# Optimization experiments

Hardware: AMD Instinct MI355X
Metric: run time of the kernel (lower is better)

## Reference

```python
import jax, jax.numpy as jnp
import numpy as np

T, B, E, H = 512, 64, 1024, 1024


def setup_inputs() -> dict:
    key = jax.random.key(0)
    ks = jax.random.split(key, 9)
    s = 1.0 / np.sqrt(E + H)  # torch Linear default init scale
    def lin(kw, kb):
        W = jax.random.uniform(kw, (H, E + H), jnp.float32, -s, s)
        b = jax.random.uniform(kb, (H,), jnp.float32, -s, s)
        return W, b
    Wf, bf = lin(ks[0], ks[1])
    Wi, bi = lin(ks[2], ks[3])
    Wo, bo = lin(ks[4], ks[5])
    Wc, bc = lin(ks[6], ks[7])
    embedding = jax.random.normal(ks[8], (T, B, E), jnp.float32)
    return {"embedding": embedding, "Wf": Wf, "bf": bf, "Wi": Wi, "bi": bi,
            "Wo": Wo, "bo": bo, "Wc": Wc, "bc": bc}


def reference(embedding, Wf, bf, Wi, bi, Wo, bo, Wc, bc):
    # embedding: [T, B, E]; each W: [H, E+H] acting on concat([x, h]).
    t, b, e = embedding.shape
    h_dim = bf.shape[0]
    # Fuse the 4 gate linears into one GEMM; split input vs hidden parts.
    Wx = jnp.concatenate([Wf[:, :e], Wi[:, :e], Wo[:, :e], Wc[:, :e]], axis=0)   # [4H, E]
    Wh = jnp.concatenate([Wf[:, e:], Wi[:, e:], Wo[:, e:], Wc[:, e:]], axis=0)   # [4H, H]
    bias = jnp.concatenate([bf, bi, bo, bc])                                      # [4H]
    # Precompute input contribution for all timesteps in one big GEMM.
    xg = jnp.einsum('tbe,ge->tbg', embedding, Wx) + bias                          # [T, B, 4H]

    def step(carry, xg_t):
        h, c = carry
        g = xg_t + h @ Wh.T                                                       # [B, 4H]
        f = jax.nn.sigmoid(g[:, :h_dim])
        i = jax.nn.sigmoid(g[:, h_dim:2 * h_dim])
        o = jax.nn.sigmoid(g[:, 2 * h_dim:3 * h_dim])
        c_tilde = jnp.tanh(g[:, 3 * h_dim:])
        c_new = f * c + i * c_tilde
        h_new = o * jnp.tanh(c_new)
        return (h_new, c_new), h_new

    h0 = jnp.zeros((b, h_dim), embedding.dtype)
    c0 = jnp.zeros((b, h_dim), embedding.dtype)
    _, hs = jax.lax.scan(step, (h0, c0), xg)                                      # [T, B, H]
    return jnp.transpose(hs, (1, 0, 2))                                           # [B, T, H] (torch.stack dim=1)
```

## Files before the change

### kernel.cpp

```cpp
#include <hip/hip_runtime.h>
#include <stdint.h>

#define T_DIM 512
#define B_DIM 64
#define E_DIM 1024
#define H_DIM 1024
#define G_DIM 4096
#define SBLK 256
#define CPB  64

typedef short bf16x8 __attribute__((ext_vector_type(8)));
typedef float f32x4 __attribute__((ext_vector_type(4)));

__device__ __forceinline__ unsigned short f2b(float f){
  union{float f; unsigned u;} v; v.f = f;
  unsigned r = (v.u + 0x7FFFu + ((v.u >> 16) & 1u)) >> 16;
  return (unsigned short)r;
}
__device__ __forceinline__ float b2f(unsigned short u){
  union{unsigned u; float f;} v; v.u = ((unsigned)u) << 16; return v.f;
}
__device__ __forceinline__ float fsigmoid(float x){
  return 1.f / (1.f + __expf(-x));
}
__device__ __forceinline__ float ftanh(float x){
  return 2.f / (1.f + __expf(-2.f * x)) - 1.f;
}

template<int OFF>
__device__ __forceinline__ bf16x8 ld_h16(const unsigned short* p){
  bf16x8 r;
  asm volatile("global_load_dwordx4 %0, %1, off offset:%2 sc0 sc1"
               : "=v"(r) : "v"(p), "i"(OFF) : "memory");
  return r;
}
__device__ __forceinline__ bf16x8 ld_g16(const unsigned short* p){
  bf16x8 r;
  asm volatile("global_load_dwordx4 %0, %1, off"
               : "=v"(r) : "v"(p) : "memory");
  return r;
}

#define LD8(dst, base, K0) \
  dst[0]=ld_h16<((K0)+0)*64>(base); dst[1]=ld_h16<((K0)+1)*64>(base); \
  dst[2]=ld_h16<((K0)+2)*64>(base); dst[3]=ld_h16<((K0)+3)*64>(base); \
  dst[4]=ld_h16<((K0)+4)*64>(base); dst[5]=ld_h16<((K0)+5)*64>(base); \
  dst[6]=ld_h16<((K0)+6)*64>(base); dst[7]=ld_h16<((K0)+7)*64>(base);

#define WAITV(N) \
  asm volatile("s_waitcnt vmcnt(" #N ")" ::: "memory"); \
  __builtin_amdgcn_sched_barrier(0x100);

#define MFMA_GRP(buf, G) \
  { _Pragma("unroll") \
    for (int u = 0; u < 8; ++u){ \
      int kc_ = (G)*8 + u; \
      bf16x8 b0 = *(const bf16x8*)&Wl[((0*32 + kc_)*64 + lane)*8]; \
      bf16x8 b1 = *(const bf16x8*)&Wl[((1*32 + kc_)*64 + lane)*8]; \
      bf16x8 b2 = *(const bf16x8*)&Wl[((2*32 + kc_)*64 + lane)*8]; \
      bf16x8 b3 = *(const bf16x8*)&Wl[((3*32 + kc_)*64 + lane)*8]; \
      acc0 = __builtin_amdgcn_mfma_f32_16x16x32_bf16(buf[u], b0, acc0, 0,0,0); \
      acc1 = __builtin_amdgcn_mfma_f32_16x16x32_bf16(buf[u], b1, acc1, 0,0,0); \
      acc2 = __builtin_amdgcn_mfma_f32_16x16x32_bf16(buf[u], b2, acc2, 0,0,0); \
      acc3 = __builtin_amdgcn_mfma_f32_16x16x32_bf16(buf[u], b3, acc3, 0,0,0); \
    } }


__global__ void pack_weights(const float* __restrict__ Wf, const float* __restrict__ Wi,
                             const float* __restrict__ Wo, const float* __restrict__ Wc,
                             const float* __restrict__ bfv, const float* __restrict__ biv,
                             const float* __restrict__ bov, const float* __restrict__ bcv,
                             unsigned short* __restrict__ WxB, unsigned short* __restrict__ WhB,
                             float* __restrict__ biasP){
  int p = blockIdx.x;
  int j = p >> 2, g = p & 3;
  const float* W    = (g==0)?Wf:(g==1)?Wi:(g==2)?Wo:Wc;
  const float* bsrc = (g==0)?bfv:(g==1)?biv:(g==2)?bov:bcv;
  const float* wrow = W + (size_t)j * 2048;
  int t = threadIdx.x;
  float4 x = *(const float4*)(wrow + 4*t);
  float4 h = *(const float4*)(wrow + 1024 + 4*t);
  ushort4 xo = make_ushort4(f2b(x.x), f2b(x.y), f2b(x.z), f2b(x.w));
  ushort4 ho = make_ushort4(f2b(h.x), f2b(h.y), f2b(h.z), f2b(h.w));
  *(ushort4*)&WxB[(size_t)p*1024 + 4*t] = xo;
  *(ushort4*)&WhB[(size_t)p*1024 + 4*t] = ho;
  if (t == 0) biasP[p] = bsrc[j];
}

__global__ void conv_emb(const float* __restrict__ emb, unsigned short* __restrict__ embB,
                         size_t n4){
  for (size_t i = (size_t)blockIdx.x * blockDim.x + threadIdx.x; i < n4;
       i += (size_t)gridDim.x * blockDim.x){
    float4 v = ((const float4*)emb)[i];
    ((ushort4*)embB)[i] = make_ushort4(f2b(v.x), f2b(v.y), f2b(v.z), f2b(v.w));
  }
}

__global__ void zero_state(unsigned short* __restrict__ h0, unsigned short* __restrict__ h1,
                           float* __restrict__ c, int* __restrict__ flags){
  int i = blockIdx.x * blockDim.x + threadIdx.x;
  h0[i] = 0; h1[i] = 0; c[i] = 0.f;
  if (i < SBLK * 16) flags[i] = 0;
}

__launch_bounds__(256)
__global__ void gemm_xg(const unsigned short* __restrict__ A,
                        const unsigned short* __restrict__ B,
                        unsigned short* __restrict__ C){
  __shared__ unsigned short Al[128*32];
  __shared__ unsigned short Bl[128*32];
  int m0 = blockIdx.x * 128, n0 = blockIdx.y * 128;
  int tid = threadIdx.x, lane = tid & 63, wid = tid >> 6;
  int mblk = (wid >> 1) * 64, nblk = (wid & 1) * 64;
  int rl = lane & 15, kg = lane >> 4;
  f32x4 acc[4][4] = {};

  for (int kk = 0; kk < 1024; kk += 32){
    {
      int c0 = tid, c1 = tid + 256;
      int r = c0 >> 2, g = c0 & 3, s = g ^ ((r >> 1) & 3);
      *(uint4*)&Al[r*32 + s*8] = *(const uint4*)&A[(size_t)(m0 + r)*1024 + kk + g*8];
      *(uint4*)&Bl[r*32 + s*8] = *(const uint4*)&B[(size_t)(n0 + r)*1024 + kk + g*8];
      r = c1 >> 2; g = c1 & 3; s = g ^ ((r >> 1) & 3);
      *(uint4*)&Al[r*32 + s*8] = *(const uint4*)&A[(size_t)(m0 + r)*1024 + kk + g*8];
      *(uint4*)&Bl[r*32 + s*8] = *(const uint4*)&B[(size_t)(n0 + r)*1024 + kk + g*8];
    }
    __syncthreads();
    bf16x8 a[4], b[4];
    #pragma unroll
    for (int mf = 0; mf < 4; ++mf){
      int r = mblk + mf*16 + rl;
      a[mf] = *(const bf16x8*)&Al[r*32 + (kg ^ ((r >> 1) & 3))*8];
    }
    #pragma unroll
    for (int nf = 0; nf < 4; ++nf){
      int r = nblk + nf*16 + rl;
      b[nf] = *(const bf16x8*)&Bl[r*32 + (kg ^ ((r >> 1) & 3))*8];
    }
    #pragma unroll
    for (int mf = 0; mf < 4; ++mf)
      #pragma unroll
      for (int nf = 0; nf < 4; ++nf)
        acc[mf][nf] = __builtin_amdgcn_mfma_f32_16x16x32_bf16(a[mf], b[nf], acc[mf][nf], 0, 0, 0);
    __syncthreads();
  }

  int rq = kg * 4;
  #pragma unroll
  for (int mf = 0; mf < 4; ++mf)
    #pragma unroll
    for (int nf = 0; nf < 4; ++nf){
      int col = n0 + nblk + nf*16 + rl;
      #pragma unroll
      for (int r = 0; r < 4; ++r){
        int row = m0 + mblk + mf*16 + rq + r;
        C[(size_t)row * G_DIM + col] = f2b(acc[mf][nf][r]);
      }
    }
}

__launch_bounds__(64, 1)
__global__ void lstm_scan(const unsigned short* __restrict__ WhB,
                          const unsigned short* __restrict__ xgc,
                          const float* __restrict__ biasP,
                          unsigned short* __restrict__ hb0,
                          unsigned short* __restrict__ hb1,
                          float* __restrict__ cglob,
                          float* __restrict__ out,
                          int* __restrict__ flags,
                          int t0, int t1){
  __shared__ unsigned short Wl[4*32*64*8];
  __shared__ float gl[16][68];

  const int tid = threadIdx.x;
  const int blk = blockIdx.x;
  const int cs = blk >> 2, rq = blk & 3;
  const int lane = tid;
  const int rl = lane & 15, kg = lane >> 4;

  for (int idx = tid; idx < 4*32*64; idx += 64){
    int ct = idx >> 11, kc = (idx >> 6) & 31, l = idx & 63;
    int col = cs*CPB + ct*16 + (l & 15);
    int k   = kc*32 + (l >> 4)*8;
    *(bf16x8*)&Wl[idx*8] = *(const bf16x8*)&WhB[(size_t)col*1024 + k];
  }

  const int bb = tid >> 2, q = tid & 3, cb = q * 16;
  const int rowg = rq*16 + bb;
  const int jb = cs*16 + q*4;
  f32x4 bias[4];
  #pragma unroll
  for (int p = 0; p < 4; ++p)
    bias[p] = *(const f32x4*)&biasP[cs*CPB + cb + p*4];
  f32x4 cv = *(const f32x4*)&cglob[(size_t)rowg*H_DIM + jb];

  const int* fpoll = &flags[(4*lane + rq) * 16];

  __syncthreads();
  asm volatile("s_waitcnt vmcnt(0)" ::: "memory");

  for (int t = t0; t < t1; ++t){
    const unsigned short* hin = (t & 1) ? hb1 : hb0;
    unsigned short* hout = (t & 1) ? hb0 : hb1;

    const unsigned short* xgp = xgc + ((size_t)(t - t0)*B_DIM + rowg)*G_DIM + cs*CPB + cb;
    const unsigned short* ap  = hin + (size_t)(rq*16 + rl)*1024 + kg*8;
    bf16x8 xr0 = ld_g16(xgp);
    bf16x8 xr1 = ld_g16(xgp + 8);
    bf16x8 aA[8], aB[8], aC[8], aD[8];
    LD8(aA, ap, 0);  LD8(aB, ap, 8);  LD8(aC, ap, 16);  LD8(aD, ap, 24);

    f32x4 acc0 = {}, acc1 = {}, acc2 = {}, acc3 = {};
    WAITV(24);
    MFMA_GRP(aA, 0);
    WAITV(16);
    MFMA_GRP(aB, 1);
    WAITV(8);
    MFMA_GRP(aC, 2);
    WAITV(0);
    MFMA_GRP(aD, 3);

    {
      int r0 = kg * 4;
      #pragma unroll
      for (int r = 0; r < 4; ++r){
        gl[r0 + r][ 0 + rl] = acc0[r];
        gl[r0 + r][16 + rl] = acc1[r];
        gl[r0 + r][32 + rl] = acc2[r];
        gl[r0 + r][48 + rl] = acc3[r];
      }
    }
    __syncthreads();

    union { ushort4 s; unsigned long long qq; } hu;
    f32x4 ov;
    {
      f32x4 g0, g1, g2, g3;
      #pragma unroll
      for (int e = 0; e < 4; ++e){
        g0[e] = gl[bb][cb +  0 + e] + b2f(xr0[e])     + bias[0][e];
        g1[e] = gl[bb][cb +  4 + e] + b2f(xr0[4 + e]) + bias[1][e];
        g2[e] = gl[bb][cb +  8 + e] + b2f(xr1[e])     + bias[2][e];
        g3[e] = gl[bb][cb + 12 + e] + b2f(xr1[4 + e]) + bias[3][e];
      }
      float f, i_, o, ct_, hn;
      f = fsigmoid(g0[0]); i_ = fsigmoid(g0[1]); o = fsigmoid(g0[2]); ct_ = ftanh(g0[3]);
      cv[0] = f*cv[0] + i_*ct_; hn = o*ftanh(cv[0]); hu.s.x = f2b(hn); ov[0] = hn;
      f = fsigmoid(g1[0]); i_ = fsigmoid(g1[1]); o = fsigmoid(g1[2]); ct_ = ftanh(g1[3]);
      cv[1] = f*cv[1] + i_*ct_; hn = o*ftanh(cv[1]); hu.s.y = f2b(hn); ov[1] = hn;
      f = fsigmoid(g2[0]); i_ = fsigmoid(g2[1]); o = fsigmoid(g2[2]); ct_ = ftanh(g2[3]);
      cv[2] = f*cv[2] + i_*ct_; hn = o*ftanh(cv[2]); hu.s.z = f2b(hn); ov[2] = hn;
      f = fsigmoid(g3[0]); i_ = fsigmoid(g3[1]); o = fsigmoid(g3[2]); ct_ = ftanh(g3[3]);
      cv[3] = f*cv[3] + i_*ct_; hn = o*ftanh(cv[3]); hu.s.w = f2b(hn); ov[3] = hn;
    }
    __hip_atomic_store((unsigned long long*)&hout[(size_t)rowg*H_DIM + jb], hu.qq,
                       __ATOMIC_RELAXED, __HIP_MEMORY_SCOPE_AGENT);
    *(f32x4*)&out[((size_t)rowg*T_DIM + t)*H_DIM + jb] = ov;

    if (t + 1 < t1){
      asm volatile("s_waitcnt vmcnt(0)" ::: "memory");
      __syncthreads();
      if (tid == 0)
        __hip_atomic_store(&flags[blk * 16], t + 1,
                           __ATOMIC_RELAXED, __HIP_MEMORY_SCOPE_AGENT);
      {
        const int target = t + 1;
        while (__hip_atomic_load(fpoll, __ATOMIC_RELAXED, __HIP_MEMORY_SCOPE_AGENT) < target)
          __builtin_amdgcn_s_sleep(1);
      }
      __syncthreads();
      asm volatile("" ::: "memory");
    }
  }

  *(f32x4*)&cglob[(size_t)rowg*H_DIM + jb] = cv;
}

__device__ __forceinline__ bf16x8 cvt_f8(const float* p){
  float4 u = *(const float4*)p;
  float4 v = *(const float4*)(p + 4);
  bf16x8 r;
  r[0] = (short)f2b(u.x); r[1] = (short)f2b(u.y); r[2] = (short)f2b(u.z); r[3] = (short)f2b(u.w);
  r[4] = (short)f2b(v.x); r[5] = (short)f2b(v.y); r[6] = (short)f2b(v.z); r[7] = (short)f2b(v.w);
  return r;
}

__launch_bounds__(256)
__global__ void lstm_step(const unsigned short* __restrict__ WhB,
                          const unsigned short* __restrict__ WxB,
                          const float* __restrict__ emb_t,
                          const unsigned short* __restrict__ h_in,
                          unsigned short* __restrict__ h_out,
                          float* __restrict__ cbuf,
                          const float* __restrict__ biasP,
                          float* __restrict__ out, int t){
  __shared__ float glds[64 * 17];
  int tid = threadIdx.x, lane = tid & 63, w = tid >> 6;
  int blk = blockIdx.x;
  int rl = lane & 15, kg = lane >> 4;
  int arow = w * 16 + rl;
  int pcol = blk * 16 + rl;

  f32x4 acc0 = {}, acc1 = {};
  const unsigned short* hrow = h_in + (size_t)arow * 1024 + kg * 8;
  const unsigned short* wrow = WhB + (size_t)pcol * 1024 + kg * 8;
  #pragma unroll 4
  for (int kk = 0; kk < 1024; kk += 64){
    bf16x8 a0 = *(const bf16x8*)(hrow + kk);
    bf16x8 b0 = *(const bf16x8*)(wrow + kk);
    bf16x8 a1 = *(const bf16x8*)(hrow + kk + 32);
    bf16x8 b1 = *(const bf16x8*)(wrow + kk + 32);
    acc0 = __builtin_amdgcn_mfma_f32_16x16x32_bf16(a0, b0, acc0, 0, 0, 0);
    acc1 = __builtin_amdgcn_mfma_f32_16x16x32_bf16(a1, b1, acc1, 0, 0, 0);
  }
  {
    const float* xrow = emb_t + (size_t)arow * 1024 + kg * 8;
    const unsigned short* wxrow = WxB + (size_t)pcol * 1024 + kg * 8;
    #pragma unroll 4
    for (int kk = 0; kk < 1024; kk += 64){
      bf16x8 a0 = cvt_f8(xrow + kk);
      bf16x8 b0 = *(const bf16x8*)(wxrow + kk);
      bf16x8 a1 = cvt_f8(xrow + kk + 32);
      bf16x8 b1 = *(const bf16x8*)(wxrow + kk + 32);
      acc0 = __builtin_amdgcn_mfma_f32_16x16x32_bf16(a0, b0, acc0, 0, 0, 0);
      acc1 = __builtin_amdgcn_mfma_f32_16x16x32_bf16(a1, b1, acc1, 0, 0, 0);
    }
  }
  f32x4 acc = acc0 + acc1;

  #pragma unroll
  for (int r = 0; r < 4; ++r){
    int brow = w * 16 + kg * 4 + r;
    glds[brow * 17 + rl] = acc[r];
  }
  __syncthreads();

  int b = tid >> 2, jj = tid & 3;
  int j = blk * 4 + jj;
  int pbase = blk * 16 + jj * 4;
  float gf = glds[b*17 + jj*4 + 0] + biasP[pbase + 0];
  float gi = glds[b*17 + jj*4 + 1] + biasP[pbase + 1];
  float go = glds[b*17 + jj*4 + 2] + biasP[pbase + 2];
  float gc = glds[b*17 + jj*4 + 3] + biasP[pbase + 3];
  float f  = fsigmoid(gf);
  float i_ = fsigmoid(gi);
  float o  = fsigmoid(go);
  float ct = ftanh(gc);
  float c_old = cbuf[b * H_DIM + j];
  float cn = f * c_old + i_ * ct;
  float hn = o * ftanh(cn);
  cbuf[b * H_DIM + j] = cn;
  h_out[b * H_DIM + j] = f2b(hn);
  out[((size_t)b * T_DIM + t) * H_DIM + j] = hn;
}

extern "C" void kernel_launch(void* const* d_in, const int* in_sizes, int n_in,
                              void* d_out, int out_size, void* d_ws, size_t ws_size,
                              hipStream_t stream){
  (void)in_sizes; (void)n_in; (void)out_size;
  const float* emb = (const float*)d_in[0];
  const float* Wf  = (const float*)d_in[1];
  const float* bfv = (const float*)d_in[2];
  const float* Wi  = (const float*)d_in[3];
  const float* biv = (const float*)d_in[4];
  const float* Wo  = (const float*)d_in[5];
  const float* bov = (const float*)d_in[6];
  const float* Wc  = (const float*)d_in[7];
  const float* bcv = (const float*)d_in[8];
  float* out = (float*)d_out;

  char* ws = (char*)d_ws;
  size_t off = 0;
  auto alloc = [&](size_t bytes) -> void* {
    void* p = ws + off; off += (bytes + 255) & ~(size_t)255; return p;
  };
  unsigned short* WxB   = (unsigned short*)alloc((size_t)G_DIM * 1024 * 2);
  unsigned short* WhB   = (unsigned short*)alloc((size_t)G_DIM * 1024 * 2);
  float*          biasP = (float*)alloc((size_t)G_DIM * 4);
  unsigned short* h0    = (unsigned short*)alloc((size_t)B_DIM * H_DIM * 2);
  unsigned short* h1    = (unsigned short*)alloc((size_t)B_DIM * H_DIM * 2);
  float*          cglob = (float*)alloc((size_t)B_DIM * H_DIM * 4);
  int*            flags = (int*)alloc((size_t)SBLK * 16 * 4);
  size_t base_end = off;

  int Tc = 0;
  const int cands[6] = {512, 256, 128, 64, 32, 16};
  for (int ci = 0; ci < 6; ++ci){
    size_t need = base_end
                + (size_t)cands[ci] * B_DIM * E_DIM * 2
                + (size_t)cands[ci] * B_DIM * G_DIM * 2
                + 4096;
    if (ws_size >= need){ Tc = cands[ci]; break; }
  }
  unsigned short* embB = nullptr;
  unsigned short* xgc  = nullptr;
  if (Tc > 0){
    embB = (unsigned short*)alloc((size_t)Tc * B_DIM * E_DIM * 2);
    xgc  = (unsigned short*)alloc((size_t)Tc * B_DIM * G_DIM * 2);
  }

  pack_weights<<<G_DIM, 256, 0, stream>>>(Wf, Wi, Wo, Wc, bfv, biv, bov, bcv, WxB, WhB, biasP);
  zero_state<<<256, 256, 0, stream>>>(h0, h1, cglob, flags);

  if (Tc > 0){
    for (int t0 = 0; t0 < T_DIM; t0 += Tc){
      conv_emb<<<2048, 256, 0, stream>>>(emb + (size_t)t0 * B_DIM * E_DIM, embB,
                                         (size_t)Tc * B_DIM * E_DIM / 4);
      gemm_xg<<<dim3(Tc * B_DIM / 128, G_DIM / 128), 256, 0, stream>>>(embB, WxB, xgc);
      lstm_scan<<<SBLK, 64, 0, stream>>>(WhB, xgc, biasP, h0, h1, cglob, out,
                                         flags, t0, t0 + Tc);
    }
  } else {
    for (int t = 0; t < T_DIM; ++t){
      const unsigned short* hin = (t & 1) ? h1 : h0;
      unsigned short*      hout = (t & 1) ? h0 : h1;
      lstm_step<<<256, 256, 0, stream>>>(
          WhB, WxB, emb + (size_t)t * B_DIM * E_DIM, hin, hout, cglob, biasP, out, t);
    }
  }
}
```

Before: 2.966 ms.

## Replace flag barrier with sentinel-tagged triple-buffered hidden state polling

Removes the per-step flag store/poll barrier between blocks. Hidden state is kept in a triple buffer whose slots are pre-filled with a bf16 sentinel, and consumers spin-reload only the h chunks that still hold the sentinel, so data arrival itself serves as the signal. Each block also resets its slice of the next buffer to the sentinel, and the xg loads for the next step are issued early. The aim is to cut cross-block synchronisation latency on the serial recurrence. The cost is extra polling reloads, and correctness depends on no real h value ever equalling the sentinel pattern and on ordering across the three buffers. Initial state handling when T is split into chunks also looks fragile, since only the first two buffers are seeded with the sentinel.

```diff
diff --git a/kernel.cpp b/kernel.cpp
--- a/kernel.cpp
+++ b/kernel.cpp
@@ -12,6 +12,9 @@
 typedef short bf16x8 __attribute__((ext_vector_type(8)));
 typedef float f32x4 __attribute__((ext_vector_type(4)));
 
+#define SENT16 0xFF80u
+#define SENT64 0xFF80FF80FF80FF80ULL
+
 __device__ __forceinline__ unsigned short f2b(float f){
   union{float f; unsigned u;} v; v.f = f;
   unsigned r = (v.u + 0x7FFFu + ((v.u >> 16) & 1u)) >> 16;
@@ -41,15 +44,22 @@
   return r;
 }
 
-#define LD8(dst, base, K0) \
-  dst[0]=ld_h16<((K0)+0)*64>(base); dst[1]=ld_h16<((K0)+1)*64>(base); \
-  dst[2]=ld_h16<((K0)+2)*64>(base); dst[3]=ld_h16<((K0)+3)*64>(base); \
-  dst[4]=ld_h16<((K0)+4)*64>(base); dst[5]=ld_h16<((K0)+5)*64>(base); \
-  dst[6]=ld_h16<((K0)+6)*64>(base); dst[7]=ld_h16<((K0)+7)*64>(base);
-
-#define WAITV(N) \
-  asm volatile("s_waitcnt vmcnt(" #N ")" ::: "memory"); \
-  __builtin_amdgcn_sched_barrier(0x100);
+#define RELOAD8(mask, dst, base, K0) \
+  if(((mask)>>0)&1u) dst[0]=ld_h16<((K0)+0)*64>(base); \
+  if(((mask)>>1)&1u) dst[1]=ld_h16<((K0)+1)*64>(base); \
+  if(((mask)>>2)&1u) dst[2]=ld_h16<((K0)+2)*64>(base); \
+  if(((mask)>>3)&1u) dst[3]=ld_h16<((K0)+3)*64>(base); \
+  if(((mask)>>4)&1u) dst[4]=ld_h16<((K0)+4)*64>(base); \
+  if(((mask)>>5)&1u) dst[5]=ld_h16<((K0)+5)*64>(base); \
+  if(((mask)>>6)&1u) dst[6]=ld_h16<((K0)+6)*64>(base); \
+  if(((mask)>>7)&1u) dst[7]=ld_h16<((K0)+7)*64>(base);
+
+#define CHECK8(mask, dst) { \
+  mask = 0; \
+  _Pragma("unroll") \
+  for (int f_ = 0; f_ < 8; ++f_) \
+    mask |= (unsigned)(((unsigned short)dst[f_][0]) == SENT16 || \
+                       ((unsigned short)dst[f_][4]) == SENT16) << f_; }
 
 #define MFMA_GRP(buf, G) \
   { _Pragma("unroll") \
@@ -96,11 +106,14 @@
   }
 }
 
-__global__ void zero_state(unsigned short* __restrict__ h0, unsigned short* __restrict__ h1,
-                           float* __restrict__ c, int* __restrict__ flags){
+__global__ void zero_state(unsigned short* __restrict__ hbuf,
+                           float* __restrict__ c, int scan_mode){
   int i = blockIdx.x * blockDim.x + threadIdx.x;
-  h0[i] = 0; h1[i] = 0; c[i] = 0.f;
-  if (i < SBLK * 16) flags[i] = 0;
+  unsigned short s = scan_mode ? (unsigned short)SENT16 : (unsigned short)0;
+  hbuf[i] = s;
+  hbuf[i + B_DIM*H_DIM] = s;
+  hbuf[i + 2*B_DIM*H_DIM] = 0;
+  c[i] = 0.f;
 }
 
 __launch_bounds__(256)
@@ -163,11 +176,9 @@
 __global__ void lstm_scan(const unsigned short* __restrict__ WhB,
                           const unsigned short* __restrict__ xgc,
                           const float* __restrict__ biasP,
-                          unsigned short* __restrict__ hb0,
-                          unsigned short* __restrict__ hb1,
+                          unsigned short* __restrict__ hbuf,
                           float* __restrict__ cglob,
                           float* __restrict__ out,
-                          int* __restrict__ flags,
                           int t0, int t1){
   __shared__ unsigned short Wl[4*32*64*8];
   __shared__ float gl[16][68];
@@ -194,30 +205,40 @@
     bias[p] = *(const f32x4*)&biasP[cs*CPB + cb + p*4];
   f32x4 cv = *(const f32x4*)&cglob[(size_t)rowg*H_DIM + jb];
 
-  const int* fpoll = &flags[(4*lane + rq) * 16];
-
   __syncthreads();
-  asm volatile("s_waitcnt vmcnt(0)" ::: "memory");
+
+  const unsigned short* xgp0 = xgc + ((size_t)0*B_DIM + rowg)*G_DIM + cs*CPB + cb;
+  bf16x8 xr0 = ld_g16(xgp0);
+  bf16x8 xr1 = ld_g16(xgp0 + 8);
 
   for (int t = t0; t < t1; ++t){
-    const unsigned short* hin = (t & 1) ? hb1 : hb0;
-    unsigned short* hout = (t & 1) ? hb0 : hb1;
-
-    const unsigned short* xgp = xgc + ((size_t)(t - t0)*B_DIM + rowg)*G_DIM + cs*CPB + cb;
-    const unsigned short* ap  = hin + (size_t)(rq*16 + rl)*1024 + kg*8;
-    bf16x8 xr0 = ld_g16(xgp);
-    bf16x8 xr1 = ld_g16(xgp + 8);
+    const unsigned short* hin  = hbuf + (size_t)((t + 2) % 3) * B_DIM * H_DIM;
+    unsigned short*       hout = hbuf + (size_t)( t      % 3) * B_DIM * H_DIM;
+    unsigned short*       hrst = hbuf + (size_t)((t + 1) % 3) * B_DIM * H_DIM;
+
+    const unsigned short* ap = hin + (size_t)(rq*16 + rl)*1024 + kg*8;
     bf16x8 aA[8], aB[8], aC[8], aD[8];
-    LD8(aA, ap, 0);  LD8(aB, ap, 8);  LD8(aC, ap, 16);  LD8(aD, ap, 24);
+    unsigned mA = 0xFFu, mB = 0xFFu, mC = 0xFFu, mD = 0xFFu;
+    for (int pass = 0; pass < 8192; ++pass){
+      RELOAD8(mA, aA, ap, 0);
+      RELOAD8(mB, aB, ap, 8);
+      RELOAD8(mC, aC, ap, 16);
+      RELOAD8(mD, aD, ap, 24);
+      asm volatile("s_waitcnt vmcnt(0)" ::: "memory");
+      __builtin_amdgcn_sched_barrier(0);
+      CHECK8(mA, aA); CHECK8(mB, aB); CHECK8(mC, aC); CHECK8(mD, aD);
+      if (!__any((mA | mB | mC | mD) != 0u)) break;
+      __builtin_amdgcn_s_sleep(1);
+    }
+
+    __hip_atomic_store(
+        (unsigned long long*)&hrst[(size_t)(rq*16 + rl)*H_DIM + cs*16 + kg*4],
+        SENT64, __ATOMIC_RELAXED, __HIP_MEMORY_SCOPE_AGENT);
 
     f32x4 acc0 = {}, acc1 = {}, acc2 = {}, acc3 = {};
-    WAITV(24);
     MFMA_GRP(aA, 0);
-    WAITV(16);
     MFMA_GRP(aB, 1);
-    WAITV(8);
     MFMA_GRP(aC, 2);
-    WAITV(0);
     MFMA_GRP(aD, 3);
 
     {
@@ -253,24 +274,17 @@
       f = fsigmoid(g3[0]); i_ = fsigmoid(g3[1]); o = fsigmoid(g3[2]); ct_ = ftanh(g3[3]);
       cv[3] = f*cv[3] + i_*ct_; hn = o*ftanh(cv[3]); hu.s.w = f2b(hn); ov[3] = hn;
     }
+
+    asm volatile("s_waitcnt vmcnt(0)" ::: "memory");
     __hip_atomic_store((unsigned long long*)&hout[(size_t)rowg*H_DIM + jb], hu.qq,
                        __ATOMIC_RELAXED, __HIP_MEMORY_SCOPE_AGENT);
     *(f32x4*)&out[((size_t)rowg*T_DIM + t)*H_DIM + jb] = ov;
-
     if (t + 1 < t1){
-      asm volatile("s_waitcnt vmcnt(0)" ::: "memory");
-      __syncthreads();
-      if (tid == 0)
-        __hip_atomic_store(&flags[blk * 16], t + 1,
-                           __ATOMIC_RELAXED, __HIP_MEMORY_SCOPE_AGENT);
-      {
-        const int target = t + 1;
-        while (__hip_atomic_load(fpoll, __ATOMIC_RELAXED, __HIP_MEMORY_SCOPE_AGENT) < target)
-          __builtin_amdgcn_s_sleep(1);
-      }
-      __syncthreads();
-      asm volatile("" ::: "memory");
-    }
+      const unsigned short* xgp = xgc + ((size_t)(t + 1 - t0)*B_DIM + rowg)*G_DIM + cs*CPB + cb;
+      xr0 = ld_g16(xgp);
+      xr1 = ld_g16(xgp + 8);
+    }
+    __syncthreads();
   }
 
   *(f32x4*)&cglob[(size_t)rowg*H_DIM + jb] = cv;
@@ -377,10 +391,8 @@
   unsigned short* WxB   = (unsigned short*)alloc((size_t)G_DIM * 1024 * 2);
   unsigned short* WhB   = (unsigned short*)alloc((size_t)G_DIM * 1024 * 2);
   float*          biasP = (float*)alloc((size_t)G_DIM * 4);
-  unsigned short* h0    = (unsigned short*)alloc((size_t)B_DIM * H_DIM * 2);
-  unsigned short* h1    = (unsigned short*)alloc((size_t)B_DIM * H_DIM * 2);
+  unsigned short* hbuf  = (unsigned short*)alloc((size_t)3 * B_DIM * H_DIM * 2);
   float*          cglob = (float*)alloc((size_t)B_DIM * H_DIM * 4);
-  int*            flags = (int*)alloc((size_t)SBLK * 16 * 4);
   size_t base_end = off;
 
   int Tc = 0;
@@ -400,17 +412,19 @@
   }
 
   pack_weights<<<G_DIM, 256, 0, stream>>>(Wf, Wi, Wo, Wc, bfv, biv, bov, bcv, WxB, WhB, biasP);
-  zero_state<<<256, 256, 0, stream>>>(h0, h1, cglob, flags);
+  zero_state<<<256, 256, 0, stream>>>(hbuf, cglob, Tc > 0 ? 1 : 0);
 
   if (Tc > 0){
     for (int t0 = 0; t0 < T_DIM; t0 += Tc){
       conv_emb<<<2048, 256, 0, stream>>>(emb + (size_t)t0 * B_DIM * E_DIM, embB,
                                          (size_t)Tc * B_DIM * E_DIM / 4);
       gemm_xg<<<dim3(Tc * B_DIM / 128, G_DIM / 128), 256, 0, stream>>>(embB, WxB, xgc);
-      lstm_scan<<<SBLK, 64, 0, stream>>>(WhB, xgc, biasP, h0, h1, cglob, out,
-                                         flags, t0, t0 + Tc);
+      lstm_scan<<<SBLK, 64, 0, stream>>>(WhB, xgc, biasP, hbuf, cglob, out,
+                                         t0, t0 + Tc);
     }
   } else {
+    unsigned short* h0 = hbuf;
+    unsigned short* h1 = hbuf + (size_t)B_DIM * H_DIM;
     for (int t = 0; t < T_DIM; ++t){
       const unsigned short* hin = (t & 1) ? h1 : h0;
       unsigned short*      hout = (t & 1) ? h0 : h1;
```

Measured after the change: 3.763 ms. 1.27x slower.

## Restructure LSTM scan into 64 blocks with two-phase batch-half pipelining

Applied to the files above, without the earlier changes.

The persistent scan kernel now runs 64 blocks instead of 256. Each block covers all 64 batch rows, split into two halves of 32 that alternate phases, so one half's MFMA work overlaps the other half's flag wait and prefetch of h and xg. The block-wide barrier plus single flag is replaced by per-half flags, wave-level __any polling, and non-blocking flag prefetch, with asm-level stores and tuned vmcnt waits. This is meant to cut grid-wide synchronisation cost and expose latency hiding across the recurrence. The cost is fewer CUs in use and fragile hand-counted waitcnt sequencing.

```diff
diff --git a/kernel.cpp b/kernel.cpp
--- a/kernel.cpp
+++ b/kernel.cpp
@@ -6,7 +6,7 @@
 #define E_DIM 1024
 #define H_DIM 1024
 #define G_DIM 4096
-#define SBLK 256
+#define SBLK 64
 #define CPB  64
 
 typedef short bf16x8 __attribute__((ext_vector_type(8)));
@@ -40,18 +40,40 @@
                : "=v"(r) : "v"(p) : "memory");
   return r;
 }
-
-#define LD8(dst, base, K0) \
-  dst[0]=ld_h16<((K0)+0)*64>(base); dst[1]=ld_h16<((K0)+1)*64>(base); \
-  dst[2]=ld_h16<((K0)+2)*64>(base); dst[3]=ld_h16<((K0)+3)*64>(base); \
-  dst[4]=ld_h16<((K0)+4)*64>(base); dst[5]=ld_h16<((K0)+5)*64>(base); \
-  dst[6]=ld_h16<((K0)+6)*64>(base); dst[7]=ld_h16<((K0)+7)*64>(base);
+__device__ __forceinline__ void st_h16(unsigned short* p, bf16x8 v){
+  asm volatile("global_store_dwordx4 %0, %1, off sc0 sc1"
+               :: "v"(p), "v"(v) : "memory");
+}
+__device__ __forceinline__ void st_g16(float* p, f32x4 v){
+  asm volatile("global_store_dwordx4 %0, %1, off"
+               :: "v"(p), "v"(v) : "memory");
+}
+__device__ __forceinline__ void st_flag(int* p, int v){
+  asm volatile("global_store_dword %0, %1, off sc0 sc1"
+               :: "v"(p), "v"(v) : "memory");
+}
+__device__ __forceinline__ int ld_flag_nb(const int* p){
+  int r;
+  asm volatile("global_load_dword %0, %1, off sc0 sc1"
+               : "=v"(r) : "v"(p) : "memory");
+  return r;
+}
 
 #define WAITV(N) \
   asm volatile("s_waitcnt vmcnt(" #N ")" ::: "memory"); \
   __builtin_amdgcn_sched_barrier(0x100);
 
-#define MFMA_GRP(buf, G) \
+#define LD16(d0, d1, p0, p1, G) \
+  d0[0]=ld_h16<((G)*8+0)*64>(p0); d0[1]=ld_h16<((G)*8+1)*64>(p0); \
+  d0[2]=ld_h16<((G)*8+2)*64>(p0); d0[3]=ld_h16<((G)*8+3)*64>(p0); \
+  d0[4]=ld_h16<((G)*8+4)*64>(p0); d0[5]=ld_h16<((G)*8+5)*64>(p0); \
+  d0[6]=ld_h16<((G)*8+6)*64>(p0); d0[7]=ld_h16<((G)*8+7)*64>(p0); \
+  d1[0]=ld_h16<((G)*8+0)*64>(p1); d1[1]=ld_h16<((G)*8+1)*64>(p1); \
+  d1[2]=ld_h16<((G)*8+2)*64>(p1); d1[3]=ld_h16<((G)*8+3)*64>(p1); \
+  d1[4]=ld_h16<((G)*8+4)*64>(p1); d1[5]=ld_h16<((G)*8+5)*64>(p1); \
+  d1[6]=ld_h16<((G)*8+6)*64>(p1); d1[7]=ld_h16<((G)*8+7)*64>(p1);
+
+#define MFMA_GRP2(a0, a1, G) \
   { _Pragma("unroll") \
     for (int u = 0; u < 8; ++u){ \
       int kc_ = (G)*8 + u; \
@@ -59,10 +81,14 @@
       bf16x8 b1 = *(const bf16x8*)&Wl[((1*32 + kc_)*64 + lane)*8]; \
       bf16x8 b2 = *(const bf16x8*)&Wl[((2*32 + kc_)*64 + lane)*8]; \
       bf16x8 b3 = *(const bf16x8*)&Wl[((3*32 + kc_)*64 + lane)*8]; \
-      acc0 = __builtin_amdgcn_mfma_f32_16x16x32_bf16(buf[u], b0, acc0, 0,0,0); \
-      acc1 = __builtin_amdgcn_mfma_f32_16x16x32_bf16(buf[u], b1, acc1, 0,0,0); \
-      acc2 = __builtin_amdgcn_mfma_f32_16x16x32_bf16(buf[u], b2, acc2, 0,0,0); \
-      acc3 = __builtin_amdgcn_mfma_f32_16x16x32_bf16(buf[u], b3, acc3, 0,0,0); \
+      acc00 = __builtin_amdgcn_mfma_f32_16x16x32_bf16(a0[u], b0, acc00, 0,0,0); \
+      acc01 = __builtin_amdgcn_mfma_f32_16x16x32_bf16(a0[u], b1, acc01, 0,0,0); \
+      acc02 = __builtin_amdgcn_mfma_f32_16x16x32_bf16(a0[u], b2, acc02, 0,0,0); \
+      acc03 = __builtin_amdgcn_mfma_f32_16x16x32_bf16(a0[u], b3, acc03, 0,0,0); \
+      acc10 = __builtin_amdgcn_mfma_f32_16x16x32_bf16(a1[u], b0, acc10, 0,0,0); \
+      acc11 = __builtin_amdgcn_mfma_f32_16x16x32_bf16(a1[u], b1, acc11, 0,0,0); \
+      acc12 = __builtin_amdgcn_mfma_f32_16x16x32_bf16(a1[u], b2, acc12, 0,0,0); \
+      acc13 = __builtin_amdgcn_mfma_f32_16x16x32_bf16(a1[u], b3, acc13, 0,0,0); \
     } }
 
 
@@ -100,7 +126,7 @@
                            float* __restrict__ c, int* __restrict__ flags){
   int i = blockIdx.x * blockDim.x + threadIdx.x;
   h0[i] = 0; h1[i] = 0; c[i] = 0.f;
-  if (i < SBLK * 16) flags[i] = 0;
+  if (i < 4096) flags[i] = 0;
 }
 
 __launch_bounds__(256)
@@ -159,6 +185,70 @@
     }
 }
 
+#define PHASE(G, t)                                                            \
+{                                                                              \
+             \
+  WAITV(18);        \
+  st_flag(&flags[(cs*2 + ((G)^1))*16], ((G)==0) ? (t) : ((t)+1));              \
+  f32x4 acc00={},acc01={},acc02={},acc03={},acc10={},acc11={},acc12={},acc13={};\
+  MFMA_GRP2(P0, P1, 0);                                                        \
+  LD16(P0, P1, ap0, ap1, 2);                    \
+  LD16(R0, R1, ap0, ap1, 3);                                                   \
+  pv = ld_flag_nb(&flags[(lane*2 + ((G)^1))*16]);                              \
+  WAITV(35);                                                \
+  MFMA_GRP2(Q0, Q1, 1);                                                        \
+  WAITV(17);                                                \
+  MFMA_GRP2(P0, P1, 2);                                                        \
+  WAITV(1);                               \
+  MFMA_GRP2(R0, R1, 3);                                                        \
+  asm volatile("s_waitcnt lgkmcnt(0)" ::: "memory");                           \
+  { int r0 = kg*4;                                                             \
+    _Pragma("unroll") for (int rg = 0; rg < 4; ++rg){                          \
+      gl[r0+rg][ 0+rl]=acc00[rg]; gl[r0+rg][16+rl]=acc01[rg];                  \
+      gl[r0+rg][32+rl]=acc02[rg]; gl[r0+rg][48+rl]=acc03[rg];                  \
+      gl[16+r0+rg][ 0+rl]=acc10[rg]; gl[16+r0+rg][16+rl]=acc11[rg];            \
+      gl[16+r0+rg][32+rl]=acc12[rg]; gl[16+r0+rg][48+rl]=acc13[rg]; } }        \
+  asm volatile("s_waitcnt lgkmcnt(0)" ::: "memory");                           \
+  __builtin_amdgcn_sched_barrier(0);                                           \
+  union{ unsigned short us[8]; bf16x8 v; } hp;                                 \
+  f32x4 ovA, ovB;                                                              \
+  _Pragma("unroll") for (int m = 0; m < 8; ++m){                               \
+    f32x4 gv = *(const f32x4*)&gl[bb][q*32 + m*4];                             \
+    _Pragma("unroll") for (int e = 0; e < 4; ++e)                              \
+      gv[e] += b2f((unsigned short)xr[m>>1][(m&1)*4 + e]) + bias8[m][e];       \
+    float f_ = fsigmoid(gv[0]), i_ = fsigmoid(gv[1]);                          \
+    float o_ = fsigmoid(gv[2]), ct_ = ftanh(gv[3]);                            \
+    float c_ = f_*cvs[G][m] + i_*ct_; cvs[G][m] = c_;                          \
+    float hn = o_*ftanh(c_);                                                   \
+    hp.us[m] = f2b(hn);                                                        \
+    if (m < 4) ovA[m] = hn; else ovB[m-4] = hn;                                \
+  }                                                                            \
+  { unsigned short* hout = ((t)&1) ? hb0 : hb1;                                \
+    st_h16(&hout[(size_t)((G)*32 + bb)*H_DIM + cs*16 + q*8], hp.v); }          \
+  WAITV(1);                              \
+  __builtin_amdgcn_sched_barrier(0);                                           \
+  { const int tn = ((G)==0) ? (t) : ((t)+1);                                   \
+    if (__any(pv < tn)){          \
+      const int* fp = &flags[(lane*2 + ((G)^1))*16];                           \
+      while (__any(__hip_atomic_load(fp, __ATOMIC_RELAXED,                     \
+                                     __HIP_MEMORY_SCOPE_AGENT) < tn))          \
+        __builtin_amdgcn_s_sleep(1);                                           \
+    }                                                                          \
+    const unsigned short* hinN = ((tn)&1) ? hb1 : hb0;                         \
+    ap0 = hinN + (size_t)((((G)^1)*32) + rl)*1024 + kg*8;                      \
+    ap1 = ap0 + (size_t)16*1024;                                               \
+    int txg = (tn < t1) ? tn : (t1 - 1);                                       \
+    const unsigned short* xgpN = xgc + ((size_t)(txg - t0)*B_DIM               \
+        + (((G)^1)*32 + bb))*G_DIM + cs*64 + q*32;                             \
+    xr[0] = ld_g16(xgpN);      xr[1] = ld_g16(xgpN + 8);                       \
+    xr[2] = ld_g16(xgpN + 16); xr[3] = ld_g16(xgpN + 24);                      \
+    LD16(P0, P1, ap0, ap1, 0);                                                 \
+    LD16(Q0, Q1, ap0, ap1, 1);                                                 \
+    st_g16(&out[((size_t)((G)*32 + bb)*T_DIM + (t))*H_DIM + cs*16 + q*8], ovA);\
+    st_g16(&out[((size_t)((G)*32 + bb)*T_DIM + (t))*H_DIM + cs*16 + q*8 + 4], ovB);\
+  }                                                                            \
+}
+
 __launch_bounds__(64, 1)
 __global__ void lstm_scan(const unsigned short* __restrict__ WhB,
                           const unsigned short* __restrict__ xgc,
@@ -170,11 +260,10 @@
                           int* __restrict__ flags,
                           int t0, int t1){
   __shared__ unsigned short Wl[4*32*64*8];
-  __shared__ float gl[16][68];
+  __shared__ float gl[32][68];
 
   const int tid = threadIdx.x;
-  const int blk = blockIdx.x;
-  const int cs = blk >> 2, rq = blk & 3;
+  const int cs = blockIdx.x;
   const int lane = tid;
   const int rl = lane & 15, kg = lane >> 4;
 
@@ -185,95 +274,64 @@
     *(bf16x8*)&Wl[idx*8] = *(const bf16x8*)&WhB[(size_t)col*1024 + k];
   }
 
-  const int bb = tid >> 2, q = tid & 3, cb = q * 16;
-  const int rowg = rq*16 + bb;
-  const int jb = cs*16 + q*4;
-  f32x4 bias[4];
+  const int bb = tid >> 1, q = tid & 1;
+  f32x4 bias8[8];
   #pragma unroll
-  for (int p = 0; p < 4; ++p)
-    bias[p] = *(const f32x4*)&biasP[cs*CPB + cb + p*4];
-  f32x4 cv = *(const f32x4*)&cglob[(size_t)rowg*H_DIM + jb];
-
-  const int* fpoll = &flags[(4*lane + rq) * 16];
+  for (int m = 0; m < 8; ++m)
+    bias8[m] = *(const f32x4*)&biasP[cs*64 + q*32 + m*4];
+  float cvs[2][8];
+  #pragma unroll
+  for (int g = 0; g < 2; ++g){
+    f32x4 lo = *(const f32x4*)&cglob[(size_t)(g*32 + bb)*H_DIM + cs*16 + q*8];
+    f32x4 hi = *(const f32x4*)&cglob[(size_t)(g*32 + bb)*H_DIM + cs*16 + q*8 + 4];
+    #pragma unroll
+    for (int e = 0; e < 4; ++e){ cvs[g][e] = lo[e]; cvs[g][4+e] = hi[e]; }
+  }
 
   __syncthreads();
-  asm volatile("s_waitcnt vmcnt(0)" ::: "memory");
+
+  {
+    const int* fp = &flags[(lane*2 + 0)*16];
+    while (__any(__hip_atomic_load(fp, __ATOMIC_RELAXED,
+                                   __HIP_MEMORY_SCOPE_AGENT) < t0))
+      __builtin_amdgcn_s_sleep(1);
+  }
+
+  bf16x8 P0[8], P1[8], Q0[8], Q1[8], R0[8], R1[8];
+  bf16x8 xr[4];
+  const unsigned short* ap0;
+  const unsigned short* ap1;
+  int pv = 0x7FFFFFFF;
+
+  {
+    const unsigned short* hin0 = (t0 & 1) ? hb1 : hb0;
+    ap0 = hin0 + (size_t)rl*1024 + kg*8;
+    ap1 = ap0 + (size_t)16*1024;
+    bf16x8 d1 = ld_g16(xgc);
+    const unsigned short* xgp0 = xgc + ((size_t)bb)*G_DIM + cs*64 + q*32;
+    xr[0] = ld_g16(xgp0);      xr[1] = ld_g16(xgp0 + 8);
+    xr[2] = ld_g16(xgp0 + 16); xr[3] = ld_g16(xgp0 + 24);
+    LD16(P0, P1, ap0, ap1, 0);
+    LD16(Q0, Q1, ap0, ap1, 1);
+    bf16x8 d2 = ld_g16(xgc); bf16x8 d3 = ld_g16(xgc + 8);
+    asm volatile("" :: "v"(d1), "v"(d2), "v"(d3));
+  }
 
   for (int t = t0; t < t1; ++t){
-    const unsigned short* hin = (t & 1) ? hb1 : hb0;
-    unsigned short* hout = (t & 1) ? hb0 : hb1;
-
-    const unsigned short* xgp = xgc + ((size_t)(t - t0)*B_DIM + rowg)*G_DIM + cs*CPB + cb;
-    const unsigned short* ap  = hin + (size_t)(rq*16 + rl)*1024 + kg*8;
-    bf16x8 xr0 = ld_g16(xgp);
-    bf16x8 xr1 = ld_g16(xgp + 8);
-    bf16x8 aA[8], aB[8], aC[8], aD[8];
-    LD8(aA, ap, 0);  LD8(aB, ap, 8);  LD8(aC, ap, 16);  LD8(aD, ap, 24);
-
-    f32x4 acc0 = {}, acc1 = {}, acc2 = {}, acc3 = {};
-    WAITV(24);
-    MFMA_GRP(aA, 0);
-    WAITV(16);
-    MFMA_GRP(aB, 1);
-    WAITV(8);
-    MFMA_GRP(aC, 2);
-    WAITV(0);
-    MFMA_GRP(aD, 3);
-
-    {
-      int r0 = kg * 4;
-      #pragma unroll
-      for (int r = 0; r < 4; ++r){
-        gl[r0 + r][ 0 + rl] = acc0[r];
-        gl[r0 + r][16 + rl] = acc1[r];
-        gl[r0 + r][32 + rl] = acc2[r];
-        gl[r0 + r][48 + rl] = acc3[r];
-      }
-    }
-    __syncthreads();
-
-    union { ushort4 s; unsigned long long qq; } hu;
-    f32x4 ov;
-    {
-      f32x4 g0, g1, g2, g3;
-      #pragma unroll
-      for (int e = 0; e < 4; ++e){
-        g0[e] = gl[bb][cb +  0 + e] + b2f(xr0[e])     + bias[0][e];
-        g1[e] = gl[bb][cb +  4 + e] + b2f(xr0[4 + e]) + bias[1][e];
-        g2[e] = gl[bb][cb +  8 + e] + b2f(xr1[e])     + bias[2][e];
-        g3[e] = gl[bb][cb + 12 + e] + b2f(xr1[4 + e]) + bias[3][e];
-      }
-      float f, i_, o, ct_, hn;
-      f = fsigmoid(g0[0]); i_ = fsigmoid(g0[1]); o = fsigmoid(g0[2]); ct_ = ftanh(g0[3]);
-      cv[0] = f*cv[0] + i_*ct_; hn = o*ftanh(cv[0]); hu.s.x = f2b(hn); ov[0] = hn;
-      f = fsigmoid(g1[0]); i_ = fsigmoid(g1[1]); o = fsigmoid(g1[2]); ct_ = ftanh(g1[3]);
-      cv[1] = f*cv[1] + i_*ct_; hn = o*ftanh(cv[1]); hu.s.y = f2b(hn); ov[1] = hn;
-      f = fsigmoid(g2[0]); i_ = fsigmoid(g2[1]); o = fsigmoid(g2[2]); ct_ = ftanh(g2[3]);
-      cv[2] = f*cv[2] + i_*ct_; hn = o*ftanh(cv[2]); hu.s.z = f2b(hn); ov[2] = hn;
-      f = fsigmoid(g3[0]); i_ = fsigmoid(g3[1]); o = fsigmoid(g3[2]); ct_ = ftanh(g3[3]);
-      cv[3] = f*cv[3] + i_*ct_; hn = o*ftanh(cv[3]); hu.s.w = f2b(hn); ov[3] = hn;
-    }
-    __hip_atomic_store((unsigned long long*)&hout[(size_t)rowg*H_DIM + jb], hu.qq,
-                       __ATOMIC_RELAXED, __HIP_MEMORY_SCOPE_AGENT);
-    *(f32x4*)&out[((size_t)rowg*T_DIM + t)*H_DIM + jb] = ov;
-
-    if (t + 1 < t1){
-      asm volatile("s_waitcnt vmcnt(0)" ::: "memory");
-      __syncthreads();
-      if (tid == 0)
-        __hip_atomic_store(&flags[blk * 16], t + 1,
-                           __ATOMIC_RELAXED, __HIP_MEMORY_SCOPE_AGENT);
-      {
-        const int target = t + 1;
-        while (__hip_atomic_load(fpoll, __ATOMIC_RELAXED, __HIP_MEMORY_SCOPE_AGENT) < target)
-          __builtin_amdgcn_s_sleep(1);
-      }
-      __syncthreads();
-      asm volatile("" ::: "memory");
-    }
-  }
-
-  *(f32x4*)&cglob[(size_t)rowg*H_DIM + jb] = cv;
+    PHASE(0, t);
+    PHASE(1, t);
+  }
+
+  WAITV(0);
+  st_flag(&flags[(cs*2 + 1)*16], t1);
+  #pragma unroll
+  for (int g = 0; g < 2; ++g){
+    f32x4 lo, hi;
+    #pragma unroll
+    for (int e = 0; e < 4; ++e){ lo[e] = cvs[g][e]; hi[e] = cvs[g][4+e]; }
+    *(f32x4*)&cglob[(size_t)(g*32 + bb)*H_DIM + cs*16 + q*8] = lo;
+    *(f32x4*)&cglob[(size_t)(g*32 + bb)*H_DIM + cs*16 + q*8 + 4] = hi;
+  }
 }
 
 __device__ __forceinline__ bf16x8 cvt_f8(const float* p){
@@ -380,7 +438,7 @@
   unsigned short* h0    = (unsigned short*)alloc((size_t)B_DIM * H_DIM * 2);
   unsigned short* h1    = (unsigned short*)alloc((size_t)B_DIM * H_DIM * 2);
   float*          cglob = (float*)alloc((size_t)B_DIM * H_DIM * 4);
-  int*            flags = (int*)alloc((size_t)SBLK * 16 * 4);
+  int*            flags = (int*)alloc((size_t)4096 * 4);
   size_t base_end = off;
 
   int Tc = 0;
```

New measurement: 6.112 ms, median of 4. 106% more time.
